# Performance work log

Hardware: AMD Instinct MI355X
Metric: run time of the kernel (lower is better)

Reference implementation:

```python
import jax, jax.numpy as jnp
import numpy as np

N_HEADS = 16

def setup_inputs() -> dict:
    key = jax.random.key(0)
    k1, k2, k3, k4 = jax.random.split(key, 4)
    B, N, E = 4, 2048, 1024
    x = jax.random.normal(k1, (B, N, E), dtype=jnp.float32)
    s = 1.0 / np.sqrt(E)
    Wq = jax.random.normal(k2, (E, E), dtype=jnp.float32) * s
    Wk = jax.random.normal(k3, (E, E), dtype=jnp.float32) * s
    Wv = jax.random.normal(k4, (E, E), dtype=jnp.float32) * s
    return {"x": x, "Wq": Wq, "Wk": Wk, "Wv": Wv}

def reference(x, Wq, Wk, Wv):
    # first_block=False -> PositionalEncoding is identity: encoded_vectors = x
    B, N, E = x.shape
    H = N_HEADS
    D = E // H
    norm = np.sqrt(D).astype(np.float32)
    # torch nn.Linear(bias=False): y = x @ W.T
    q = (x @ Wq.T).reshape(B, N, H, D).transpose(0, 2, 1, 3)  # [B,H,N,D]
    k = (x @ Wk.T).reshape(B, N, H, D).transpose(0, 2, 1, 3)
    v = (x @ Wv.T).reshape(B, N, H, D).transpose(0, 2, 1, 3)
    scores = jnp.einsum('bhnd,bhmd->bhnm', q, k) / norm  # [B,H,N,N]
    attn = jax.nn.softmax(scores, axis=-1)
    # original einsum 'stuu, stuv -> stuv': diagonal of attn scales values
    diag = jnp.diagonal(attn, axis1=-2, axis2=-1)  # [B,H,N]
    av = diag[..., None] * v  # [B,H,N,D]
    av = av.transpose(0, 2, 1, 3).reshape(B, N, E)
    return (av, x)
```

## Files before the change

### kernel.cpp

```cpp
#include <hip/hip_runtime.h>
#include <hip/hip_bf16.h>
#include <stdint.h>

typedef __attribute__((ext_vector_type(8))) short short8;
typedef __attribute__((ext_vector_type(4))) float f32x4;

#define BATCH 4
#define SEQ   2048
#define EMB   1024
#define HEADS 16
#define DHEAD 64
#define MROWS (BATCH * SEQ)
#define NW    (EMB * EMB)

#define QSCALE 0.18033688011112042f

__device__ inline unsigned short f2bf(float f) {
    unsigned int u = __float_as_uint(f);
    unsigned int r = (u + 0x7fffu + ((u >> 16) & 1u)) >> 16;
    return (unsigned short)r;
}

__device__ __forceinline__ void gl_lds16(const short* g, short* l) {
    __builtin_amdgcn_global_load_lds(
        (const __attribute__((address_space(1))) void*)g,
        (__attribute__((address_space(3))) void*)l, 16, 0, 0);
}

template <int N>
__device__ __forceinline__ void waitvm() {
    asm volatile("s_waitcnt vmcnt(%0)" :: "n"(N) : "memory");
}

__global__ __launch_bounds__(256) void pack_all(const float* __restrict__ x,
                                                const float* __restrict__ wq,
                                                const float* __restrict__ wk,
                                                const float* __restrict__ wv,
                                                unsigned short* __restrict__ xb,
                                                unsigned short* __restrict__ wb,
                                                float* __restrict__ pass) {
    const int i = (blockIdx.x * 256 + threadIdx.x) * 8;
    const float* src;
    unsigned short* dst;
    bool isx = i < MROWS * EMB;
    if (isx) {
        src = x + i;
        dst = xb + i;
    } else {
        const int j = i - MROWS * EMB;
        src = (j < NW) ? wq + j : (j < 2 * NW) ? wk + (j - NW) : wv + (j - 2 * NW);
        dst = wb + j;
    }
    const float4* s = reinterpret_cast<const float4*>(src);
    float4 f0 = s[0];
    float4 f1 = s[1];
    union { unsigned short u[8]; short8 v; } o;
    o.u[0] = f2bf(f0.x); o.u[1] = f2bf(f0.y); o.u[2] = f2bf(f0.z); o.u[3] = f2bf(f0.w);
    o.u[4] = f2bf(f1.x); o.u[5] = f2bf(f1.y); o.u[6] = f2bf(f1.z); o.u[7] = f2bf(f1.w);
    *reinterpret_cast<short8*>(dst) = o.v;
    if (isx) {
        float4* p = reinterpret_cast<float4*>(pass + i);
        p[0] = f0;
        p[1] = f1;
    }
}

template <int MODE>
__global__ __launch_bounds__(512, 2) void gemm8(const short* __restrict__ A,
                                                const short* __restrict__ Bm,
                                                unsigned short* __restrict__ Cb,
                                                float* __restrict__ out,
                                                const float* __restrict__ num,
                                                const float* __restrict__ pp) {
    constexpr int K = EMB;
    constexpr int NT = K / 32;
    constexpr int BN = (MODE == 0) ? 256 : 128;
    constexpr int NF = BN / 64;
    constexpr int BUFSTRIDE = 8192 + BN * 32;
    constexpr int VW = 2 + BN / 128;

    __shared__ short Ks[3 * BUFSTRIDE];

    const int t = threadIdx.x;
    const int lane = t & 63;
    const int w = t >> 6;
    const int wr = w >> 2;
    const int wc = w & 3;
    const int rl = lane & 15;
    const int pg = (lane >> 4) ^ (lane & 3);
    const int m0 = blockIdx.x * 256;
    const int n0 = blockIdx.y * BN;

    const int sr = t >> 2;
    const int sg = (t & 3) ^ (sr & 3);
    const int soff = sr * K + sg * 8;
    const short* gA0 = A + (size_t)(m0)*K + soff;
    const short* gA1 = A + (size_t)(m0 + 128) * K + soff;
    const short* gB0 = Bm + (size_t)(n0)*K + soff;
    const short* gB1 = Bm + (size_t)(n0 + 128) * K + soff;
    short* ldsw = Ks + w * 512;

#define STAGE8(kk, bb)                                               \
    {                                                                \
        const int _k = (kk)*32;                                      \
        short* _l = ldsw + (bb)*BUFSTRIDE;                           \
        gl_lds16(gA0 + _k, _l);                                      \
        gl_lds16(gA1 + _k, _l + 4096);                               \
        gl_lds16(gB0 + _k, _l + 8192);                               \
        if (MODE == 0) gl_lds16(gB1 + _k, _l + 12288);               \
    }

    f32x4 acc[8][NF] = {};

    STAGE8(0, 0);
    STAGE8(1, 1);
    waitvm<VW>();
    __builtin_amdgcn_s_barrier();

    int cur = 0;
    for (int kt = 0; kt < NT; ++kt) {
        const int pf = kt + 2;
        if (pf < NT) {
            int nb = cur + 2; if (nb >= 3) nb -= 3;
            STAGE8(pf, nb);
        }

        const short* bufp = Ks + cur * BUFSTRIDE;
        short8 av[8], bv[NF];
#pragma unroll
        for (int i = 0; i < 8; i++)
            av[i] = *(const short8*)&bufp[wr * 4096 + i * 512 + rl * 32 + pg * 8];
#pragma unroll
        for (int j = 0; j < NF; j++) {
            const int brow = (MODE == 0) ? ((wc & 1) * 64 + j * 16 + rl)
                                         : (wc * 32 + j * 16 + rl);
            const int bh = (MODE == 0) ? (wc >> 1) : 0;
            bv[j] = *(const short8*)&bufp[8192 + bh * 4096 + brow * 32 + pg * 8];
        }

        __builtin_amdgcn_s_setprio(1);
#pragma unroll
        for (int i = 0; i < 8; i++)
#pragma unroll
            for (int j = 0; j < NF; j++)
                acc[i][j] = __builtin_amdgcn_mfma_f32_16x16x32_bf16(av[i], bv[j], acc[i][j], 0, 0, 0);
        __builtin_amdgcn_s_setprio(0);

        if (kt < NT - 2) waitvm<VW>();
        else             waitvm<0>();
        __builtin_amdgcn_s_barrier();

        cur += 1; if (cur == 3) cur = 0;
    }
#undef STAGE8

    const int gr_base = m0 + wr * 128 + (lane >> 4) * 4;
    const int gc_base = n0 + wc * (BN / 4) + rl;
#pragma unroll
    for (int i = 0; i < 8; i++) {
#pragma unroll
        for (int j = 0; j < NF; j++) {
            const int col = gc_base + j * 16;
#pragma unroll
            for (int r = 0; r < 4; r++) {
                const int grow = gr_base + i * 16 + r;
                const int bb = grow >> 11;
                const int nn = grow & 2047;
                if (MODE == 0) {
                    const int sel = col >> 10;
                    const int cc = col & 1023;
                    const int hh = cc >> 6;
                    const int dd = cc & 63;
                    const float sc = sel ? 1.0f : QSCALE;
                    Cb[(((size_t)((sel << 6) + (bb << 4) + hh) * SEQ + nn) << 6) + dd] =
                        f2bf(acc[i][j][r] * sc);
                } else {
                    const int hh = col >> 6;
                    const int idx = ((bb << 4) + hh) * SEQ + nn;
                    const float d = num[idx] / (pp[idx] + pp[idx + 64 * SEQ]);
                    out[(size_t)grow * EMB + col] = acc[i][j][r] * d;
                }
            }
        }
    }
}

__global__ __launch_bounds__(512, 4) void diag_kernel(const short* __restrict__ Qh,
                                                      const short* __restrict__ Kh,
                                                      float* __restrict__ num,
                                                      float* __restrict__ pp) {
    const int n = blockIdx.x;
    const int bh = (n & 7) | ((n >> 7) << 3);
    const int qt = (n >> 3) & 7;
    const int ks = (n >> 6) & 1;
    __shared__ short Ksd[2 * 8192];

    const int t = threadIdx.x;
    const int lane = t & 63;
    const int w = t >> 6;
    const int rl = lane & 15;
    const int g = lane >> 4;
    const int kq = g * 8;

    const short* Kbh = Kh + (size_t)bh * SEQ * DHEAD;
    const short* Qbh = Qh + (size_t)bh * SEQ * DHEAD;

    const int qbase = qt * 256 + w * 32;
    short8 a0[2], a1[2];
#pragma unroll
    for (int i = 0; i < 2; i++) {
        const int qrow = qbase + i * 16 + rl;
        a0[i] = *(const short8*)(Qbh + qrow * DHEAD + kq);
        a1[i] = *(const short8*)(Qbh + qrow * DHEAD + kq + 32);
    }

    float sdiag[2];
    const int rr = rl - g * 4;
#pragma unroll
    for (int i = 0; i < 2; i++) {
        const int krow = qbase + i * 16 + rl;
        const short8 b0d = *(const short8*)(Kbh + krow * DHEAD + kq);
        const short8 b1d = *(const short8*)(Kbh + krow * DHEAD + kq + 32);
        f32x4 cd = {};
        cd = __builtin_amdgcn_mfma_f32_16x16x32_bf16(a0[i], b0d, cd, 0, 0, 0);
        cd = __builtin_amdgcn_mfma_f32_16x16x32_bf16(a1[i], b1d, cd, 0, 0, 0);
        sdiag[i] = (rr >= 0 && rr < 4) ? cd[rr] : 0.f;
    }

    const int sr = t >> 3;
    const int sb = ((t & 7) ^ (sr & 7)) * 8;
    const short* gK0 = Kbh + (size_t)ks * (SEQ / 2) * DHEAD + sr * DHEAD + sb;
    const short* gK1 = gK0 + 64 * DHEAD;
    short* ldsw = Ksd + w * 512;

#define DSTAGE(kk, bb)                                       \
    {                                                        \
        gl_lds16(gK0 + (kk)*8192, ldsw + (bb)*8192);         \
        gl_lds16(gK1 + (kk)*8192, ldsw + (bb)*8192 + 4096);  \
    }

    const int blk0 = (g ^ (lane & 7)) * 8;
    const int blk1 = ((g + 4) ^ (lane & 7)) * 8;

    float ssum[2][4] = {};

    DSTAGE(0, 0);
    waitvm<0>();
    __builtin_amdgcn_s_barrier();

#define QKMFMA(sub, c)                                                          \
    {                                                                           \
        const short* _r = bufp + ((sub)*16 + rl) * 64;                          \
        const short8 _b0 = *(const short8*)(_r + blk0);                         \
        const short8 _b1 = *(const short8*)(_r + blk1);                         \
        c[0] = __builtin_amdgcn_mfma_f32_16x16x32_bf16(a0[0], _b0, f32x4{}, 0, 0, 0); \
        c[0] = __builtin_amdgcn_mfma_f32_16x16x32_bf16(a1[0], _b1, c[0], 0, 0, 0);    \
        c[1] = __builtin_amdgcn_mfma_f32_16x16x32_bf16(a0[1], _b0, f32x4{}, 0, 0, 0); \
        c[1] = __builtin_amdgcn_mfma_f32_16x16x32_bf16(a1[1], _b1, c[1], 0, 0, 0);    \
    }
#define EXPACC(c)                                         \
    {                                                     \
        _Pragma("unroll") for (int i = 0; i < 2; i++)     \
        _Pragma("unroll") for (int r = 0; r < 4; ++r)     \
            ssum[i][r] += __builtin_amdgcn_exp2f(c[i][r]); \
    }

    for (int kt = 0; kt < 8; ++kt) {
        if (kt < 7) DSTAGE(kt + 1, (kt + 1) & 1);
        const short* bufp = Ksd + (kt & 1) * 8192;

        f32x4 cE[2], cO[2];
        QKMFMA(0, cE);
        QKMFMA(1, cO);
        EXPACC(cE);
        QKMFMA(2, cE);
        EXPACC(cO);
        QKMFMA(3, cO);
        EXPACC(cE);
        QKMFMA(4, cE);
        EXPACC(cO);
        QKMFMA(5, cO);
        EXPACC(cE);
        QKMFMA(6, cE);
        EXPACC(cO);
        QKMFMA(7, cO);
        EXPACC(cE);
        EXPACC(cO);

        if (kt < 7) {
            waitvm<0>();
            __builtin_amdgcn_s_barrier();
        }
    }
#undef DSTAGE
#undef QKMFMA
#undef EXPACC

#pragma unroll
    for (int i = 0; i < 2; i++)
#pragma unroll
        for (int r = 0; r < 4; r++) {
            float v = ssum[i][r];
            v += __shfl_xor(v, 1);
            v += __shfl_xor(v, 2);
            v += __shfl_xor(v, 4);
            v += __shfl_xor(v, 8);
            ssum[i][r] = v;
        }

    if (rr >= 0 && rr < 4) {
#pragma unroll
        for (int i = 0; i < 2; i++) {
            const int q = qbase + i * 16 + rl;
            pp[(ks * 64 + bh) * SEQ + q] = ssum[i][rr];
            if (ks == 0) num[bh * SEQ + q] = __builtin_amdgcn_exp2f(sdiag[i]);
        }
    }
}

extern "C" void kernel_launch(void* const* d_in, const int* in_sizes, int n_in,
                              void* d_out, int out_size, void* d_ws, size_t ws_size,
                              hipStream_t stream) {
    const float* x  = (const float*)d_in[0];
    const float* Wq = (const float*)d_in[1];
    const float* Wk = (const float*)d_in[2];
    const float* Wv = (const float*)d_in[3];
    float* out = (float*)d_out;
    char* ws = (char*)d_ws;

    const size_t xb_off  = 0;
    const size_t wq_off  = xb_off + (size_t)MROWS * EMB * 2;
    const size_t wk_off  = wq_off + (size_t)NW * 2;
    const size_t wv_off  = wk_off + (size_t)NW * 2;
    const size_t q_off   = wv_off + (size_t)NW * 2;
    const size_t k_off   = q_off + (size_t)MROWS * EMB * 2;
    const size_t num_off = k_off + (size_t)MROWS * EMB * 2;
    const size_t pp_off  = num_off + (size_t)64 * SEQ * 4;

    short* xb  = (short*)(ws + xb_off);
    short* wqb = (short*)(ws + wq_off);
    short* wvb = (short*)(ws + wv_off);
    short* Qh  = (short*)(ws + q_off);
    short* Kh  = (short*)(ws + k_off);
    float* num = (float*)(ws + num_off);
    float* pp  = (float*)(ws + pp_off);

    const int npack = (MROWS * EMB + 3 * NW) / 2048;

    pack_all<<<npack, 256, 0, stream>>>(x, Wq, Wk, Wv,
                                        (unsigned short*)xb, (unsigned short*)wqb,
                                        out + (size_t)MROWS * EMB);

    gemm8<0><<<dim3(MROWS / 256, 2048 / 256), 512, 0, stream>>>(
        xb, wqb, (unsigned short*)Qh, nullptr, nullptr, nullptr);

    diag_kernel<<<1024, 512, 0, stream>>>(Qh, Kh, num, pp);

    gemm8<1><<<dim3(MROWS / 256, EMB / 128), 512, 0, stream>>>(
        xb, wvb, nullptr, out, num, pp);
}
```

Baseline: 131.1 us.

## Double per-wave query rows in diag kernel and triple-buffer K staging

The softmax-denominator kernel now gives each wave 64 query rows instead of 32, so every K tile loaded into LDS feeds twice as many MFMAs, and the grid shrinks from 1024 to 512 blocks. K staging moves from double to triple buffering with a prefetch distance of two and partial vmcnt waits, so loads overlap the math better. The diagonal-score computation now runs only in the ks==0 blocks. The cost is higher register use (more accumulators and A fragments), more LDS per block, and fewer blocks to fill the GPU.

```diff
diff --git a/kernel.cpp b/kernel.cpp
--- a/kernel.cpp
+++ b/kernel.cpp
@@ -190,10 +190,10 @@
                                                       float* __restrict__ num,
                                                       float* __restrict__ pp) {
     const int n = blockIdx.x;
-    const int bh = (n & 7) | ((n >> 7) << 3);
-    const int qt = (n >> 3) & 7;
-    const int ks = (n >> 6) & 1;
-    __shared__ short Ksd[2 * 8192];
+    const int bh = (n & 7) | ((n >> 6) << 3);
+    const int qt = (n >> 3) & 3;
+    const int ks = (n >> 5) & 1;
+    __shared__ short Ksd[3 * 8192];
 
     const int t = threadIdx.x;
     const int lane = t & 63;
@@ -205,47 +205,57 @@
     const short* Kbh = Kh + (size_t)bh * SEQ * DHEAD;
     const short* Qbh = Qh + (size_t)bh * SEQ * DHEAD;
 
-    const int qbase = qt * 256 + w * 32;
-    short8 a0[2], a1[2];
-#pragma unroll
-    for (int i = 0; i < 2; i++) {
+    const int qbase = qt * 512 + w * 64;
+    short8 a0[4], a1[4];
+#pragma unroll
+    for (int i = 0; i < 4; i++) {
         const int qrow = qbase + i * 16 + rl;
         a0[i] = *(const short8*)(Qbh + qrow * DHEAD + kq);
         a1[i] = *(const short8*)(Qbh + qrow * DHEAD + kq + 32);
     }
 
-    float sdiag[2];
     const int rr = rl - g * 4;
-#pragma unroll
-    for (int i = 0; i < 2; i++) {
-        const int krow = qbase + i * 16 + rl;
-        const short8 b0d = *(const short8*)(Kbh + krow * DHEAD + kq);
-        const short8 b1d = *(const short8*)(Kbh + krow * DHEAD + kq + 32);
-        f32x4 cd = {};
-        cd = __builtin_amdgcn_mfma_f32_16x16x32_bf16(a0[i], b0d, cd, 0, 0, 0);
-        cd = __builtin_amdgcn_mfma_f32_16x16x32_bf16(a1[i], b1d, cd, 0, 0, 0);
-        sdiag[i] = (rr >= 0 && rr < 4) ? cd[rr] : 0.f;
+
+    if (ks == 0) {
+        float sdiag[4];
+#pragma unroll
+        for (int i = 0; i < 4; i++) {
+            const int krow = qbase + i * 16 + rl;
+            const short8 b0d = *(const short8*)(Kbh + krow * DHEAD + kq);
+            const short8 b1d = *(const short8*)(Kbh + krow * DHEAD + kq + 32);
+            f32x4 cd = {};
+            cd = __builtin_amdgcn_mfma_f32_16x16x32_bf16(a0[i], b0d, cd, 0, 0, 0);
+            cd = __builtin_amdgcn_mfma_f32_16x16x32_bf16(a1[i], b1d, cd, 0, 0, 0);
+            sdiag[i] = (rr >= 0 && rr < 4) ? cd[rr] : 0.f;
+        }
+        if (rr >= 0 && rr < 4) {
+#pragma unroll
+            for (int i = 0; i < 4; i++)
+                num[bh * SEQ + qbase + i * 16 + rl] =
+                    __builtin_amdgcn_exp2f(sdiag[i]);
+        }
     }
 
     const int sr = t >> 3;
     const int sb = ((t & 7) ^ (sr & 7)) * 8;
-    const short* gK0 = Kbh + (size_t)ks * (SEQ / 2) * DHEAD + sr * DHEAD + sb;
+    const short* gK0 = Kbh + (size_t)ks * 1024 * DHEAD + sr * DHEAD + sb;
     const short* gK1 = gK0 + 64 * DHEAD;
     short* ldsw = Ksd + w * 512;
 
-#define DSTAGE(kk, bb)                                       \
-    {                                                        \
-        gl_lds16(gK0 + (kk)*8192, ldsw + (bb)*8192);         \
-        gl_lds16(gK1 + (kk)*8192, ldsw + (bb)*8192 + 4096);  \
+#define DSTAGE(kk, bb)                                        \
+    {                                                         \
+        gl_lds16(gK0 + (kk)*8192, ldsw + (bb)*8192);          \
+        gl_lds16(gK1 + (kk)*8192, ldsw + (bb)*8192 + 4096);   \
     }
 
     const int blk0 = (g ^ (lane & 7)) * 8;
     const int blk1 = ((g + 4) ^ (lane & 7)) * 8;
 
-    float ssum[2][4] = {};
+    float ssum[4][4] = {};
 
     DSTAGE(0, 0);
-    waitvm<0>();
+    DSTAGE(1, 1);
+    waitvm<2>();
     __builtin_amdgcn_s_barrier();
 
 #define QKMFMA(sub, c)                                                          \
@@ -253,23 +263,27 @@
         const short* _r = bufp + ((sub)*16 + rl) * 64;                          \
         const short8 _b0 = *(const short8*)(_r + blk0);                         \
         const short8 _b1 = *(const short8*)(_r + blk1);                         \
-        c[0] = __builtin_amdgcn_mfma_f32_16x16x32_bf16(a0[0], _b0, f32x4{}, 0, 0, 0); \
-        c[0] = __builtin_amdgcn_mfma_f32_16x16x32_bf16(a1[0], _b1, c[0], 0, 0, 0);    \
-        c[1] = __builtin_amdgcn_mfma_f32_16x16x32_bf16(a0[1], _b0, f32x4{}, 0, 0, 0); \
-        c[1] = __builtin_amdgcn_mfma_f32_16x16x32_bf16(a1[1], _b1, c[1], 0, 0, 0);    \
+        _Pragma("unroll") for (int i = 0; i < 4; i++) {                         \
+            c[i] = __builtin_amdgcn_mfma_f32_16x16x32_bf16(a0[i], _b0, f32x4{}, 0, 0, 0); \
+            c[i] = __builtin_amdgcn_mfma_f32_16x16x32_bf16(a1[i], _b1, c[i], 0, 0, 0);    \
+        }                                                                       \
     }
 #define EXPACC(c)                                         \
     {                                                     \
-        _Pragma("unroll") for (int i = 0; i < 2; i++)     \
+        _Pragma("unroll") for (int i = 0; i < 4; i++)     \
         _Pragma("unroll") for (int r = 0; r < 4; ++r)     \
             ssum[i][r] += __builtin_amdgcn_exp2f(c[i][r]); \
     }
 
+    int cur = 0;
     for (int kt = 0; kt < 8; ++kt) {
-        if (kt < 7) DSTAGE(kt + 1, (kt + 1) & 1);
-        const short* bufp = Ksd + (kt & 1) * 8192;
-
-        f32x4 cE[2], cO[2];
+        if (kt + 2 < 8) {
+            int nb = cur + 2; if (nb >= 3) nb -= 3;
+            DSTAGE(kt + 2, nb);
+        }
+        const short* bufp = Ksd + cur * 8192;
+
+        f32x4 cE[4], cO[4];
         QKMFMA(0, cE);
         QKMFMA(1, cO);
         EXPACC(cE);
@@ -288,16 +302,18 @@
         EXPACC(cO);
 
         if (kt < 7) {
-            waitvm<0>();
+            if (kt < 6) waitvm<2>();
+            else        waitvm<0>();
             __builtin_amdgcn_s_barrier();
         }
+        cur += 1; if (cur == 3) cur = 0;
     }
 #undef DSTAGE
 #undef QKMFMA
 #undef EXPACC
 
 #pragma unroll
-    for (int i = 0; i < 2; i++)
+    for (int i = 0; i < 4; i++)
 #pragma unroll
         for (int r = 0; r < 4; r++) {
             float v = ssum[i][r];
@@ -310,11 +326,8 @@
 
     if (rr >= 0 && rr < 4) {
 #pragma unroll
-        for (int i = 0; i < 2; i++) {
-            const int q = qbase + i * 16 + rl;
-            pp[(ks * 64 + bh) * SEQ + q] = ssum[i][rr];
-            if (ks == 0) num[bh * SEQ + q] = __builtin_amdgcn_exp2f(sdiag[i]);
-        }
+        for (int i = 0; i < 4; i++)
+            pp[(ks * 64 + bh) * SEQ + qbase + i * 16 + rl] = ssum[i][rr];
     }
 }
 
@@ -354,7 +367,7 @@
     gemm8<0><<<dim3(MROWS / 256, 2048 / 256), 512, 0, stream>>>(
         xb, wqb, (unsigned short*)Qh, nullptr, nullptr, nullptr);
 
-    diag_kernel<<<1024, 512, 0, stream>>>(Qh, Kh, num, pp);
+    diag_kernel<<<512, 512, 0, stream>>>(Qh, Kh, num, pp);
 
     gemm8<1><<<dim3(MROWS / 256, EMB / 128), 512, 0, stream>>>(
         xb, wvb, nullptr, out, num, pp);
```

New measurement: 349.7 us. 2.67x slower.
